# Kernel tuning notes

Hardware: AMD Instinct MI355X
Metric: run time of the kernel (lower is better)

## Reference

```python
import jax, jax.numpy as jnp
import numpy as np

D_MODEL = 1024
N_HEADS = 16
MAX_SEQ_LEN = 2048

def setup_inputs() -> dict:
    key = jax.random.key(0)
    ks = jax.random.split(key, 4)
    B, L, D = 2, 2048, D_MODEL
    s = 0.02
    x = jax.random.normal(ks[0], (B, L, D), dtype=jnp.float32)
    qkv_w = jax.random.normal(ks[1], (D, 3 * D), dtype=jnp.float32) * s
    qkv_b = jnp.zeros((3 * D,), dtype=jnp.float32)
    proj_w = jax.random.normal(ks[2], (D, D), dtype=jnp.float32) * s
    proj_b = jnp.zeros((D,), dtype=jnp.float32)
    bias_table = jax.random.normal(ks[3], (2 * MAX_SEQ_LEN - 1, N_HEADS), dtype=jnp.float32) * s
    return {"x": x, "qkv_w": qkv_w, "qkv_b": qkv_b, "proj_w": proj_w, "proj_b": proj_b, "bias_table": bias_table}

def reference(x, qkv_w, qkv_b, proj_w, proj_b, bias_table):
    B, L, D = x.shape
    H = N_HEADS
    dk = D // H
    scale = dk ** -0.5
    # fused qkv projection: (B,L,3,H,dk)
    qkv = (x @ qkv_w + qkv_b).reshape(B, L, 3, H, dk)
    q = qkv[:, :, 0].transpose(0, 2, 1, 3)  # (B,H,L,dk)
    k = qkv[:, :, 1].transpose(0, 2, 1, 3)
    v = qkv[:, :, 2].transpose(0, 2, 1, 3)
    attn = jnp.einsum("bhqd,bhkd->bhqk", q, k) * scale  # (B,H,L,L)
    # relative position bias gather (Swin-style)
    coords = jnp.arange(L)
    rel_idx = coords[None, :] - coords[:, None] + (MAX_SEQ_LEN - 1)  # (L,L)
    rel_bias = bias_table[rel_idx]  # (L,L,H)
    attn = attn + rel_bias.transpose(2, 0, 1)[None]  # (B,H,L,L)
    attn = jax.nn.softmax(attn, axis=-1)
    out = jnp.einsum("bhqk,bhkd->bhqd", attn, v)  # (B,H,L,dk)
    out = out.transpose(0, 2, 1, 3).reshape(B, L, D)
    return out @ proj_w + proj_b
```

## Files before the change

kernel.cpp:

```cpp
#include <hip/hip_runtime.h>
#include <stdint.h>

typedef __attribute__((ext_vector_type(4))) float    f32x4;
typedef f32x4 __attribute__((aligned(4)))   f32x4u;
typedef __attribute__((ext_vector_type(8))) short    bf16x8;
typedef __attribute__((ext_vector_type(2))) uint32_t u32x2;

#define MFMA16(a,b,c) __builtin_amdgcn_mfma_f32_16x16x32_bf16((a),(b),(c),0,0,0)

__device__ __forceinline__ uint16_t f2bf(float f){
  uint32_t u = __float_as_uint(f);
  return (uint16_t)((u + 0x7FFFu + ((u >> 16) & 1u)) >> 16);
}

__device__ __forceinline__ uint32_t pk_bf16(float lo, float hi){
  uint32_t r; asm("v_cvt_pk_bf16_f32 %0, %1, %2" : "=v"(r) : "v"(lo), "v"(hi)); return r;
}

__device__ __forceinline__ float fast_exp2(float x){
  float r; asm("v_exp_f32 %0, %1" : "=v"(r) : "v"(x)); return r;
}

__device__ __forceinline__ void gload16(const uint16_t* g, uint16_t* l){
  __builtin_amdgcn_global_load_lds((const __attribute__((address_space(1))) uint32_t*)g,
                                   (__attribute__((address_space(3))) uint32_t*)l, 16, 0, 0);
}

__global__ void k_prep(const float* __restrict__ x, uint16_t* __restrict__ x_bf,
                       const float* __restrict__ btab, float* __restrict__ bias_t,
                       const float* __restrict__ qkv_w, uint16_t* __restrict__ qkv_wt,
                       const float* __restrict__ proj_w, uint16_t* __restrict__ proj_wt){
  __shared__ float tile[64][65];
  const int bx = blockIdx.x;
  if (bx < 4096){
    const size_t i = (size_t)(bx*256 + threadIdx.x) * 4;
    const f32x4 v = *(const f32x4*)(x + i);
    u32x2 pk = {pk_bf16(v[0], v[1]), pk_bf16(v[2], v[3])};
    *(u32x2*)(x_bf + i) = pk;
    return;
  }
  if (bx < 4352){
    const int i = (bx - 4096)*256 + threadIdx.x;
    if (i < 4095*16) bias_t[(i & 15)*4096 + (i >> 4)] = btab[i] * 1.4426950408889634f;
    return;
  }
  const float* in;  uint16_t* out;  int K, N, n0, k0;
  if (bx < 5120){
    const int b2 = bx - 4352;
    in = qkv_w; out = qkv_wt; K = 1024; N = 3072;
    n0 = (b2 % 48)*64; k0 = (b2 / 48)*64;
  } else {
    const int b3 = bx - 5120;
    in = proj_w; out = proj_wt; K = 1024; N = 1024;
    n0 = (b3 % 16)*64; k0 = (b3 / 16)*64;
  }
  const int tc = threadIdx.x & 63, tr = threadIdx.x >> 6;
  #pragma unroll
  for (int p=0;p<16;p++){ int r = p*4 + tr; tile[r][tc] = in[(size_t)(k0+r)*N + n0 + tc]; }
  __syncthreads();
  #pragma unroll
  for (int p=0;p<16;p++){ int r = p*4 + tr; out[(size_t)(n0+r)*K + k0 + tc] = f2bf(tile[tc][r]); }
}

__global__ __launch_bounds__(256, 2) void k_gemm(
    const uint16_t* __restrict__ A, const uint16_t* __restrict__ Bt,
    const float* __restrict__ bias,
    uint16_t* __restrict__ qo, uint16_t* __restrict__ ko, uint16_t* __restrict__ vto)
{
  __shared__ __align__(16) uint16_t at[64*64];
  __shared__ __align__(16) uint16_t bt[128*64];
  const int tid = threadIdx.x;
  const int lane = tid & 63, wc = tid >> 6;
  const int g = lane >> 4, li = lane & 15;
  const int m0 = blockIdx.y * 64, n0 = blockIdx.x * 128;

  f32x4 acc[4][2] = {};

  const int srow = tid >> 3;
  const int scg  = (tid & 7) ^ (srow & 7);

  for (int kt_ = 0; kt_ < 16; kt_++){
    const int kk = kt_*64;
    __syncthreads();
    #pragma unroll
    for (int j = 0; j < 2; j++)
      gload16(A  + (size_t)(m0 + j*32 + srow)*1024 + kk + scg*8, at + (j*256+tid)*8);
    #pragma unroll
    for (int j = 0; j < 4; j++)
      gload16(Bt + (size_t)(n0 + j*32 + srow)*1024 + kk + scg*8, bt + (j*256+tid)*8);
    asm volatile("s_waitcnt vmcnt(0)" ::: "memory");
    __syncthreads();

    bf16x8 af[2][4], bfr[2][2];
    #pragma unroll
    for (int mi=0; mi<4; mi++){
      int row = mi*16 + li, sw = row & 7;
      af[0][mi] = *(const bf16x8*)(at + row*64 + ((g     ^ sw)*8));
      af[1][mi] = *(const bf16x8*)(at + row*64 + (((4+g) ^ sw)*8));
    }
    #pragma unroll
    for (int ni=0; ni<2; ni++){
      int row = wc*32 + ni*16 + li, sw = row & 7;
      bfr[0][ni] = *(const bf16x8*)(bt + row*64 + ((g     ^ sw)*8));
      bfr[1][ni] = *(const bf16x8*)(bt + row*64 + (((4+g) ^ sw)*8));
    }
    #pragma unroll
    for (int s=0; s<2; s++)
      #pragma unroll
      for (int mi=0; mi<4; mi++)
        #pragma unroll
        for (int ni=0; ni<2; ni++)
          acc[mi][ni] = MFMA16(af[s][mi], bfr[s][ni], acc[mi][ni]);
  }

  #pragma unroll
  for (int ni=0; ni<2; ni++){
    const int c = n0 + wc*32 + ni*16 + li;
    const float bv = bias[c];
    const int which = c >> 10, cc = c & 1023;
    const int h = cc >> 6, d = cc & 63;
    #pragma unroll
    for (int mi=0; mi<4; mi++){
      const int trow = m0 + mi*16 + g*4;
      const int b_ = trow >> 11, lcl = trow & 2047;
      const f32x4 v4 = acc[mi][ni];
      if (which == 0){
        uint16_t* dst = qo + (((size_t)(b_*16 + h)*2048 + lcl)*64 + d);
        #pragma unroll
        for (int r=0;r<4;r++) dst[(size_t)r*64] = f2bf((v4[r] + bv) * 0.18033688011112042f);
      } else if (which == 1){
        uint16_t* dst = ko + (((size_t)(b_*16 + h)*2048 + lcl)*64 + d);
        #pragma unroll
        for (int r=0;r<4;r++) dst[(size_t)r*64] = f2bf(v4[r] + bv);
      } else {
        u32x2 pk = {pk_bf16(v4[0]+bv, v4[1]+bv), pk_bf16(v4[2]+bv, v4[3]+bv)};
        *(u32x2*)(vto + (((size_t)(b_*16 + h)*64 + d)*2048 + lcl)) = pk;
      }
    }
  }
}

__global__ __launch_bounds__(256, 2) void k_gemm2(
    const uint16_t* __restrict__ A, const uint16_t* __restrict__ Bt,
    const float* __restrict__ bias, float* __restrict__ outf)
{
  __shared__ __align__(16) uint16_t at[128*64];
  __shared__ __align__(16) uint16_t bt[64*64];
  const int tid = threadIdx.x;
  const int lane = tid & 63, w = tid >> 6;
  const int g = lane >> 4, li = lane & 15;
  const int wr = w >> 1, wc = w & 1;
  const int m0 = blockIdx.y * 128, n0 = blockIdx.x * 64;

  f32x4 acc[4][2] = {};
  const int srow = tid >> 3;
  const int scg  = (tid & 7) ^ (srow & 7);

  for (int kt_ = 0; kt_ < 16; kt_++){
    const int kk = kt_*64;
    __syncthreads();
    #pragma unroll
    for (int j = 0; j < 4; j++)
      gload16(A  + (size_t)(m0 + j*32 + srow)*1024 + kk + scg*8, at + (j*256+tid)*8);
    #pragma unroll
    for (int j = 0; j < 2; j++)
      gload16(Bt + (size_t)(n0 + j*32 + srow)*1024 + kk + scg*8, bt + (j*256+tid)*8);
    asm volatile("s_waitcnt vmcnt(0)" ::: "memory");
    __syncthreads();

    bf16x8 af[2][4], bfr[2][2];
    #pragma unroll
    for (int mi=0; mi<4; mi++){
      int row = wr*64 + mi*16 + li, sw = row & 7;
      af[0][mi] = *(const bf16x8*)(at + row*64 + ((g     ^ sw)*8));
      af[1][mi] = *(const bf16x8*)(at + row*64 + (((4+g) ^ sw)*8));
    }
    #pragma unroll
    for (int ni=0; ni<2; ni++){
      int row = wc*32 + ni*16 + li, sw = row & 7;
      bfr[0][ni] = *(const bf16x8*)(bt + row*64 + ((g     ^ sw)*8));
      bfr[1][ni] = *(const bf16x8*)(bt + row*64 + (((4+g) ^ sw)*8));
    }
    #pragma unroll
    for (int s=0; s<2; s++)
      #pragma unroll
      for (int mi=0; mi<4; mi++)
        #pragma unroll
        for (int ni=0; ni<2; ni++)
          acc[mi][ni] = MFMA16(af[s][mi], bfr[s][ni], acc[mi][ni]);
  }

  #pragma unroll
  for (int ni=0; ni<2; ni++){
    const int c = n0 + wc*32 + ni*16 + li;
    const float bv = bias[c];
    #pragma unroll
    for (int mi=0; mi<4; mi++){
      const int trow = m0 + wr*64 + mi*16 + g*4;
      float* dst = outf + (size_t)trow*1024 + c;
      const f32x4 v4 = acc[mi][ni];
      #pragma unroll
      for (int r=0;r<4;r++) dst[(size_t)r*1024] = v4[r] + bv;
    }
  }
}

__device__ __forceinline__ void attn_tile(
    int t, bool last, int tid, int g, int li, int srow, int scg,
    const uint16_t* kbase, const uint16_t* vbase, const float* bb,
    const uint16_t* ktc, uint16_t* ktn, const uint16_t* vtc, uint16_t* vtn, uint16_t* pl,
    const bf16x8 (&qf)[2][2], bf16x8 ones,
    f32x4 (&o)[4][2], f32x4 (&o4)[2], float& mrun0, float& mrun1)
{
  const int kv0 = t*64;

  f32x4 bv5[5];
  #pragma unroll
  for (int j=0;j<5;j++)
    bv5[j] = *(const f32x4u*)(bb + kv0 + (j-1)*16 + g*4 - li);
  asm volatile("" ::: "memory");

  if (!last){
    const int kv1 = kv0 + 64;
    gload16(kbase + (size_t)(kv1+srow)*64 + scg*8,         ktn + tid*8);
    gload16(kbase + (size_t)(kv1+srow+32)*64 + scg*8,      ktn + 2048 + tid*8);
    gload16(vbase + (size_t)srow*2048 + kv1 + scg*8,       vtn + tid*8);
    gload16(vbase + (size_t)(srow+32)*2048 + kv1 + scg*8,  vtn + 2048 + tid*8);
    asm volatile("s_waitcnt vmcnt(9)" ::: "memory");
  } else {
    asm volatile("s_waitcnt vmcnt(5)" ::: "memory");
  }
  __builtin_amdgcn_s_barrier();

  f32x4 sa[4][2];
  __builtin_amdgcn_s_setprio(1);
  #pragma unroll
  for (int mf=0; mf<4; mf++){
    const int row = mf*16 + li, sw = row & 7;
    bf16x8 a0 = *(const bf16x8*)(ktc + row*64 + ((g     ^ sw)*8));
    bf16x8 a1 = *(const bf16x8*)(ktc + row*64 + (((4+g) ^ sw)*8));
    #pragma unroll
    for (int c=0;c<2;c++){
      f32x4 cfr = {};
      cfr = MFMA16(a0, qf[c][0], cfr);
      cfr = MFMA16(a1, qf[c][1], cfr);
      sa[mf][c] = cfr;
    }
  }
  __builtin_amdgcn_s_setprio(0);

  float t0 = -__builtin_inff(), t1 = -__builtin_inff();
  #pragma unroll
  for (int mf=0; mf<4; mf++){
    sa[mf][0] += bv5[mf+1];
    sa[mf][1] += bv5[mf];
    #pragma unroll
    for (int r=0; r<4; r++){
      t0 = fmaxf(t0, sa[mf][0][r]);
      t1 = fmaxf(t1, sa[mf][1][r]);
    }
  }

  const int ok = (t0 <= mrun0 + 8.f) && (t1 <= mrun1 + 8.f);
  if (!__all(ok)){
    float r0 = t0, r1 = t1;
    r0 = fmaxf(r0, __shfl_xor(r0, 16)); r0 = fmaxf(r0, __shfl_xor(r0, 32));
    r1 = fmaxf(r1, __shfl_xor(r1, 16)); r1 = fmaxf(r1, __shfl_xor(r1, 32));
    const float mn0 = fmaxf(mrun0, r0), mn1 = fmaxf(mrun1, r1);
    const float a0 = fast_exp2(mrun0 - mn0), a1 = fast_exp2(mrun1 - mn1);
    #pragma unroll
    for (int mf=0; mf<4; mf++){ o[mf][0] *= a0; o[mf][1] *= a1; }
    o4[0] *= a0; o4[1] *= a1;
    mrun0 = mn0; mrun1 = mn1;
  }

  bf16x8 av[2][4];
  #pragma unroll
  for (int s=0; s<2; s++)
    #pragma unroll
    for (int mf=0; mf<4; mf++){
      const int row = mf*16 + li, sw = row & 7;
      av[s][mf] = *(const bf16x8*)(vtc + row*64 + (((4*s+g) ^ sw)*8));
    }

  const int swp2 = 2*(li & 7);
  #pragma unroll
  for (int c=0;c<2;c++){
    const float mr = c ? mrun1 : mrun0;
    #pragma unroll
    for (int mf=0; mf<4; mf++){
      float p0 = fast_exp2(sa[mf][c][0] - mr);
      float p1 = fast_exp2(sa[mf][c][1] - mr);
      float p2 = fast_exp2(sa[mf][c][2] - mr);
      float p3 = fast_exp2(sa[mf][c][3] - mr);
      u32x2 pk = {pk_bf16(p0,p1), pk_bf16(p2,p3)};
      *(u32x2*)(pl + li*64 + (((4*mf+g) ^ swp2)*4)) = pk;
    }
    __builtin_amdgcn_s_setprio(1);
    #pragma unroll
    for (int s=0; s<2; s++){
      bf16x8 pb = *(const bf16x8*)(pl + li*64 + (((8*s+2*g) ^ swp2)*4));
      o4[c] = MFMA16(ones, pb, o4[c]);
      #pragma unroll
      for (int mf=0; mf<4; mf++)
        o[mf][c] = MFMA16(av[s][mf], pb, o[mf][c]);
    }
    __builtin_amdgcn_s_setprio(0);
  }
  __builtin_amdgcn_s_barrier();
}

__global__ __launch_bounds__(256, 2) void k_attn(
    const uint16_t* __restrict__ qg, const uint16_t* __restrict__ kg,
    const uint16_t* __restrict__ vg, const float* __restrict__ biast,
    uint16_t* __restrict__ outp)
{
  __shared__ __align__(16) uint16_t kt[2][64*64];
  __shared__ __align__(16) uint16_t vt[2][64*64];
  __shared__ __align__(16) uint16_t pt[4][16*64];
  const int tid = threadIdx.x;
  const int lane = tid & 63, w = tid >> 6;
  const int g = lane >> 4, li = lane & 15;
  const int bh = blockIdx.y, h = bh & 15, b_ = bh >> 4;
  const int qw = blockIdx.x*128 + w*32;

  bf16x8 qf[2][2];
  #pragma unroll
  for (int c=0;c<2;c++){
    const uint16_t* qp = qg + ((size_t)bh*2048 + qw + c*16 + li)*64 + g*8;
    qf[c][0] = *(const bf16x8*)(qp);
    qf[c][1] = *(const bf16x8*)(qp + 32);
  }
  bf16x8 ones = (bf16x8)(short)0;
  if (li == 0){ const short v = (short)0x3F80; ones = (bf16x8){v,v,v,v,v,v,v,v}; }

  f32x4 o[4][2] = {};
  f32x4 o4[2] = {};
  float mrun0 = -__builtin_inff(), mrun1 = -__builtin_inff();

  const uint16_t* kbase = kg + (size_t)bh*(2048*64);
  const uint16_t* vbase = vg + (size_t)bh*(64*2048);
  const int srow = tid >> 3;
  const int scg  = (tid & 7) ^ (srow & 7);
  const float* bb = biast + h*4096 + 2047 - qw;
  uint16_t* pl = &pt[w][0];

  gload16(kbase + (size_t)srow*64 + scg*8,         &kt[0][tid*8]);
  gload16(kbase + (size_t)(srow+32)*64 + scg*8,    &kt[0][2048 + tid*8]);
  gload16(vbase + (size_t)srow*2048 + scg*8,       &vt[0][tid*8]);
  gload16(vbase + (size_t)(srow+32)*2048 + scg*8,  &vt[0][2048 + tid*8]);

  for (int tt = 0; tt < 32; tt += 2){
    attn_tile(tt,   false,    tid, g, li, srow, scg, kbase, vbase, bb,
              &kt[0][0], &kt[1][0], &vt[0][0], &vt[1][0], pl,
              qf, ones, o, o4, mrun0, mrun1);
    attn_tile(tt+1, tt == 30, tid, g, li, srow, scg, kbase, vbase, bb,
              &kt[1][0], &kt[0][0], &vt[1][0], &vt[0][0], pl,
              qf, ones, o, o4, mrun0, mrun1);
  }

  const float ls0 = __shfl(o4[0][0], li);
  const float ls1 = __shfl(o4[1][0], li);
  const float inv0 = 1.0f / ls0, inv1 = 1.0f / ls1;
  #pragma unroll
  for (int c=0;c<2;c++){
    const float inv = c ? inv1 : inv0;
    const size_t token = (size_t)b_*2048 + qw + c*16 + li;
    #pragma unroll
    for (int mf=0; mf<4; mf++){
      u32x2 pk = {pk_bf16(o[mf][c][0]*inv, o[mf][c][1]*inv),
                  pk_bf16(o[mf][c][2]*inv, o[mf][c][3]*inv)};
      *(u32x2*)(outp + token*1024 + h*64 + mf*16 + g*4) = pk;
    }
  }
}

extern "C" void kernel_launch(void* const* d_in, const int* in_sizes, int n_in,
                              void* d_out, int out_size, void* d_ws, size_t ws_size,
                              hipStream_t stream)
{
  const float* x      = (const float*)d_in[0];
  const float* qkv_w  = (const float*)d_in[1];
  const float* qkv_b  = (const float*)d_in[2];
  const float* proj_w = (const float*)d_in[3];
  const float* proj_b = (const float*)d_in[4];
  const float* btab   = (const float*)d_in[5];
  float* out = (float*)d_out;

  char* p = (char*)d_ws;
  uint16_t* x_bf    = (uint16_t*)(p);
  uint16_t* qkv_wt  = (uint16_t*)(p + 8388608);
  uint16_t* proj_wt = (uint16_t*)(p + 14680064);
  uint16_t* q_buf   = (uint16_t*)(p + 16777216);
  uint16_t* k_buf   = (uint16_t*)(p + 25165824);
  uint16_t* vt_buf  = (uint16_t*)(p + 33554432);
  uint16_t* ao_buf  = (uint16_t*)(p + 41943040);
  float*    bias_t  = (float*)   (p + 50331648);

  k_prep <<<dim3(5376), dim3(256), 0, stream>>>(x, x_bf, btab, bias_t,
                                                qkv_w, qkv_wt, proj_w, proj_wt);

  k_gemm  <<<dim3(24,64), dim3(256), 0, stream>>>(x_bf, qkv_wt, qkv_b, q_buf, k_buf, vt_buf);
  k_attn  <<<dim3(16,32), dim3(256), 0, stream>>>(q_buf, k_buf, vt_buf, bias_t, ao_buf);
  k_gemm2 <<<dim3(16,32), dim3(256), 0, stream>>>(ao_buf, proj_wt, proj_b, out);
}
```

Measured before the change: 118.0 us.

## Switch attention kernel to 32x32x16 MFMA with register-resident P via cross-lane shuffles

Rewrites the attention inner loop to use 32x32x16 bf16 MFMA, so each wave computes S and O for 32 queries with two 16-wide accumulator tiles. The probabilities are repacked across the half-waves with shuffles and fed straight back as the B operand, which removes the per-wave LDS P buffer and its write/read round trip. The row sum is now accumulated in registers instead of through an extra MFMA against a ones vector. The wait counts change to match the new number of bias loads, and the register footprint per lane changes, which may affect occupancy.

```diff
diff --git a/kernel.cpp b/kernel.cpp
--- a/kernel.cpp
+++ b/kernel.cpp
@@ -1,12 +1,15 @@
 #include <hip/hip_runtime.h>
 #include <stdint.h>
 
-typedef __attribute__((ext_vector_type(4))) float    f32x4;
-typedef f32x4 __attribute__((aligned(4)))   f32x4u;
-typedef __attribute__((ext_vector_type(8))) short    bf16x8;
-typedef __attribute__((ext_vector_type(2))) uint32_t u32x2;
+typedef __attribute__((ext_vector_type(4)))  float    f32x4;
+typedef f32x4 __attribute__((aligned(4)))    f32x4u;
+typedef __attribute__((ext_vector_type(16))) float    f32x16;
+typedef __attribute__((ext_vector_type(8)))  short    bf16x8;
+typedef __attribute__((ext_vector_type(2)))  uint32_t u32x2;
+typedef __attribute__((ext_vector_type(4)))  uint32_t u32x4;
 
 #define MFMA16(a,b,c) __builtin_amdgcn_mfma_f32_16x16x32_bf16((a),(b),(c),0,0,0)
+#define MFMA32(a,b,c) __builtin_amdgcn_mfma_f32_32x32x16_bf16((a),(b),(c),0,0,0)
 
 __device__ __forceinline__ uint16_t f2bf(float f){
   uint32_t u = __float_as_uint(f);
@@ -25,6 +28,8 @@
   __builtin_amdgcn_global_load_lds((const __attribute__((address_space(1))) uint32_t*)g,
                                    (__attribute__((address_space(3))) uint32_t*)l, 16, 0, 0);
 }
+
+typedef union { u32x4 u; bf16x8 b; } pun_t;
 
 __global__ void k_prep(const float* __restrict__ x, uint16_t* __restrict__ x_bf,
                        const float* __restrict__ btab, float* __restrict__ bias_t,
@@ -206,18 +211,20 @@
 }
 
 __device__ __forceinline__ void attn_tile(
-    int t, bool last, int tid, int g, int li, int srow, int scg,
-    const uint16_t* kbase, const uint16_t* vbase, const float* bb,
-    const uint16_t* ktc, uint16_t* ktn, const uint16_t* vtc, uint16_t* vtn, uint16_t* pl,
-    const bf16x8 (&qf)[2][2], bf16x8 ones,
-    f32x4 (&o)[4][2], f32x4 (&o4)[2], float& mrun0, float& mrun1)
+    int t, bool last, int tid, int l31, int h, int srow, int scg,
+    const uint16_t* kbase, const uint16_t* vbase, const float* bbl,
+    const uint16_t* ktc, uint16_t* ktn, const uint16_t* vtc, uint16_t* vtn,
+    const bf16x8 (&qf)[4],
+    f32x16& o0, f32x16& o1, float& mrun, float& lrun)
 {
   const int kv0 = t*64;
 
-  f32x4 bv5[5];
-  #pragma unroll
-  for (int j=0;j<5;j++)
-    bv5[j] = *(const f32x4u*)(bb + kv0 + (j-1)*16 + g*4 - li);
+  f32x4 bv0[4], bv1[4];
+  #pragma unroll
+  for (int q2=0;q2<4;q2++){
+    bv0[q2] = *(const f32x4u*)(bbl + kv0 + 8*q2);
+    bv1[q2] = *(const f32x4u*)(bbl + kv0 + 32 + 8*q2);
+  }
   asm volatile("" ::: "memory");
 
   if (!last){
@@ -226,87 +233,75 @@
     gload16(kbase + (size_t)(kv1+srow+32)*64 + scg*8,      ktn + 2048 + tid*8);
     gload16(vbase + (size_t)srow*2048 + kv1 + scg*8,       vtn + tid*8);
     gload16(vbase + (size_t)(srow+32)*2048 + kv1 + scg*8,  vtn + 2048 + tid*8);
-    asm volatile("s_waitcnt vmcnt(9)" ::: "memory");
+    asm volatile("s_waitcnt vmcnt(12)" ::: "memory");
   } else {
-    asm volatile("s_waitcnt vmcnt(5)" ::: "memory");
+    asm volatile("s_waitcnt vmcnt(8)" ::: "memory");
   }
   __builtin_amdgcn_s_barrier();
 
-  f32x4 sa[4][2];
+  const int sw = l31 & 7;
+  f32x16 sA = {}, sB = {};
   __builtin_amdgcn_s_setprio(1);
   #pragma unroll
-  for (int mf=0; mf<4; mf++){
-    const int row = mf*16 + li, sw = row & 7;
-    bf16x8 a0 = *(const bf16x8*)(ktc + row*64 + ((g     ^ sw)*8));
-    bf16x8 a1 = *(const bf16x8*)(ktc + row*64 + (((4+g) ^ sw)*8));
-    #pragma unroll
-    for (int c=0;c<2;c++){
-      f32x4 cfr = {};
-      cfr = MFMA16(a0, qf[c][0], cfr);
-      cfr = MFMA16(a1, qf[c][1], cfr);
-      sa[mf][c] = cfr;
-    }
+  for (int s=0;s<4;s++){
+    const int ch = (((2*s+h) ^ sw))*8;
+    bf16x8 a0 = *(const bf16x8*)(ktc + l31*64 + ch);
+    bf16x8 a1 = *(const bf16x8*)(ktc + (32+l31)*64 + ch);
+    sA = MFMA32(a0, qf[s], sA);
+    sB = MFMA32(a1, qf[s], sB);
   }
   __builtin_amdgcn_s_setprio(0);
 
-  float t0 = -__builtin_inff(), t1 = -__builtin_inff();
-  #pragma unroll
-  for (int mf=0; mf<4; mf++){
-    sa[mf][0] += bv5[mf+1];
-    sa[mf][1] += bv5[mf];
-    #pragma unroll
-    for (int r=0; r<4; r++){
-      t0 = fmaxf(t0, sa[mf][0][r]);
-      t1 = fmaxf(t1, sa[mf][1][r]);
-    }
-  }
-
-  const int ok = (t0 <= mrun0 + 8.f) && (t1 <= mrun1 + 8.f);
+  float tmax = -__builtin_inff();
+  #pragma unroll
+  for (int r=0;r<16;r++){
+    sA[r] += bv0[r>>2][r&3];
+    sB[r] += bv1[r>>2][r&3];
+    tmax = fmaxf(tmax, fmaxf(sA[r], sB[r]));
+  }
+  tmax = fmaxf(tmax, __shfl_xor(tmax, 32));
+
+  const int ok = (tmax <= mrun + 8.f);
   if (!__all(ok)){
-    float r0 = t0, r1 = t1;
-    r0 = fmaxf(r0, __shfl_xor(r0, 16)); r0 = fmaxf(r0, __shfl_xor(r0, 32));
-    r1 = fmaxf(r1, __shfl_xor(r1, 16)); r1 = fmaxf(r1, __shfl_xor(r1, 32));
-    const float mn0 = fmaxf(mrun0, r0), mn1 = fmaxf(mrun1, r1);
-    const float a0 = fast_exp2(mrun0 - mn0), a1 = fast_exp2(mrun1 - mn1);
-    #pragma unroll
-    for (int mf=0; mf<4; mf++){ o[mf][0] *= a0; o[mf][1] *= a1; }
-    o4[0] *= a0; o4[1] *= a1;
-    mrun0 = mn0; mrun1 = mn1;
-  }
-
-  bf16x8 av[2][4];
-  #pragma unroll
-  for (int s=0; s<2; s++)
-    #pragma unroll
-    for (int mf=0; mf<4; mf++){
-      const int row = mf*16 + li, sw = row & 7;
-      av[s][mf] = *(const bf16x8*)(vtc + row*64 + (((4*s+g) ^ sw)*8));
-    }
-
-  const int swp2 = 2*(li & 7);
-  #pragma unroll
-  for (int c=0;c<2;c++){
-    const float mr = c ? mrun1 : mrun0;
-    #pragma unroll
-    for (int mf=0; mf<4; mf++){
-      float p0 = fast_exp2(sa[mf][c][0] - mr);
-      float p1 = fast_exp2(sa[mf][c][1] - mr);
-      float p2 = fast_exp2(sa[mf][c][2] - mr);
-      float p3 = fast_exp2(sa[mf][c][3] - mr);
-      u32x2 pk = {pk_bf16(p0,p1), pk_bf16(p2,p3)};
-      *(u32x2*)(pl + li*64 + (((4*mf+g) ^ swp2)*4)) = pk;
-    }
-    __builtin_amdgcn_s_setprio(1);
-    #pragma unroll
-    for (int s=0; s<2; s++){
-      bf16x8 pb = *(const bf16x8*)(pl + li*64 + (((8*s+2*g) ^ swp2)*4));
-      o4[c] = MFMA16(ones, pb, o4[c]);
-      #pragma unroll
-      for (int mf=0; mf<4; mf++)
-        o[mf][c] = MFMA16(av[s][mf], pb, o[mf][c]);
-    }
-    __builtin_amdgcn_s_setprio(0);
-  }
+    const float mn = fmaxf(mrun, tmax);
+    const float al = fast_exp2(mrun - mn);
+    #pragma unroll
+    for (int r=0;r<16;r++){ o0[r] *= al; o1[r] *= al; }
+    lrun *= al; mrun = mn;
+  }
+
+  float psum = 0.f;
+  uint32_t pkA[8], pkB[8];
+  #pragma unroll
+  for (int m=0;m<4;m++){
+    float a0 = fast_exp2(sA[4*m+0]-mrun), a1 = fast_exp2(sA[4*m+1]-mrun);
+    float a2 = fast_exp2(sA[4*m+2]-mrun), a3 = fast_exp2(sA[4*m+3]-mrun);
+    float b0 = fast_exp2(sB[4*m+0]-mrun), b1 = fast_exp2(sB[4*m+1]-mrun);
+    float b2 = fast_exp2(sB[4*m+2]-mrun), b3 = fast_exp2(sB[4*m+3]-mrun);
+    psum += ((a0+a1)+(a2+a3)) + ((b0+b1)+(b2+b3));
+    pkA[2*m] = pk_bf16(a0,a1); pkA[2*m+1] = pk_bf16(a2,a3);
+    pkB[2*m] = pk_bf16(b0,b1); pkB[2*m+1] = pk_bf16(b2,b3);
+  }
+  lrun += psum;
+
+  __builtin_amdgcn_s_setprio(1);
+  #pragma unroll
+  for (int s=0;s<4;s++){
+    const uint32_t* pks = (s < 2) ? pkA : pkB;
+    const int sl = s & 1;
+    const uint32_t c0 = pks[4*sl], c1 = pks[4*sl+1], c2 = pks[4*sl+2], c3 = pks[4*sl+3];
+    const uint32_t v0 = h ? c0 : c2, v1 = h ? c1 : c3;
+    const uint32_t r0 = (uint32_t)__shfl_xor((int)v0, 32);
+    const uint32_t r1 = (uint32_t)__shfl_xor((int)v1, 32);
+    pun_t pn;
+    pn.u = (u32x4){ h ? r0 : c0, h ? r1 : c1, h ? c2 : r0, h ? c3 : r1 };
+    const int ch = (((2*s+h) ^ sw))*8;
+    bf16x8 av0 = *(const bf16x8*)(vtc + l31*64 + ch);
+    bf16x8 av1 = *(const bf16x8*)(vtc + (32+l31)*64 + ch);
+    o0 = MFMA32(av0, pn.b, o0);
+    o1 = MFMA32(av1, pn.b, o1);
+  }
+  __builtin_amdgcn_s_setprio(0);
   __builtin_amdgcn_s_barrier();
 }
 
@@ -317,33 +312,28 @@
 {
   __shared__ __align__(16) uint16_t kt[2][64*64];
   __shared__ __align__(16) uint16_t vt[2][64*64];
-  __shared__ __align__(16) uint16_t pt[4][16*64];
   const int tid = threadIdx.x;
   const int lane = tid & 63, w = tid >> 6;
-  const int g = lane >> 4, li = lane & 15;
-  const int bh = blockIdx.y, h = bh & 15, b_ = bh >> 4;
+  const int l31 = lane & 31, h = lane >> 5;
+  const int bh = blockIdx.y, h_head = bh & 15, b_ = bh >> 4;
   const int qw = blockIdx.x*128 + w*32;
-
-  bf16x8 qf[2][2];
-  #pragma unroll
-  for (int c=0;c<2;c++){
-    const uint16_t* qp = qg + ((size_t)bh*2048 + qw + c*16 + li)*64 + g*8;
-    qf[c][0] = *(const bf16x8*)(qp);
-    qf[c][1] = *(const bf16x8*)(qp + 32);
-  }
-  bf16x8 ones = (bf16x8)(short)0;
-  if (li == 0){ const short v = (short)0x3F80; ones = (bf16x8){v,v,v,v,v,v,v,v}; }
-
-  f32x4 o[4][2] = {};
-  f32x4 o4[2] = {};
-  float mrun0 = -__builtin_inff(), mrun1 = -__builtin_inff();
+  const int q_tok = qw + l31;
+
+  bf16x8 qf[4];
+  {
+    const uint16_t* qp = qg + ((size_t)bh*2048 + q_tok)*64 + h*8;
+    #pragma unroll
+    for (int s=0;s<4;s++) qf[s] = *(const bf16x8*)(qp + s*16);
+  }
+
+  f32x16 o0 = {}, o1 = {};
+  float mrun = -__builtin_inff(), lrun = 0.f;
 
   const uint16_t* kbase = kg + (size_t)bh*(2048*64);
   const uint16_t* vbase = vg + (size_t)bh*(64*2048);
   const int srow = tid >> 3;
   const int scg  = (tid & 7) ^ (srow & 7);
-  const float* bb = biast + h*4096 + 2047 - qw;
-  uint16_t* pl = &pt[w][0];
+  const float* bbl = biast + h_head*4096 + 2047 - q_tok + 4*h;
 
   gload16(kbase + (size_t)srow*64 + scg*8,         &kt[0][tid*8]);
   gload16(kbase + (size_t)(srow+32)*64 + scg*8,    &kt[0][2048 + tid*8]);
@@ -351,27 +341,22 @@
   gload16(vbase + (size_t)(srow+32)*2048 + scg*8,  &vt[0][2048 + tid*8]);
 
   for (int tt = 0; tt < 32; tt += 2){
-    attn_tile(tt,   false,    tid, g, li, srow, scg, kbase, vbase, bb,
-              &kt[0][0], &kt[1][0], &vt[0][0], &vt[1][0], pl,
-              qf, ones, o, o4, mrun0, mrun1);
-    attn_tile(tt+1, tt == 30, tid, g, li, srow, scg, kbase, vbase, bb,
-              &kt[1][0], &kt[0][0], &vt[1][0], &vt[0][0], pl,
-              qf, ones, o, o4, mrun0, mrun1);
-  }
-
-  const float ls0 = __shfl(o4[0][0], li);
-  const float ls1 = __shfl(o4[1][0], li);
-  const float inv0 = 1.0f / ls0, inv1 = 1.0f / ls1;
-  #pragma unroll
-  for (int c=0;c<2;c++){
-    const float inv = c ? inv1 : inv0;
-    const size_t token = (size_t)b_*2048 + qw + c*16 + li;
-    #pragma unroll
-    for (int mf=0; mf<4; mf++){
-      u32x2 pk = {pk_bf16(o[mf][c][0]*inv, o[mf][c][1]*inv),
-                  pk_bf16(o[mf][c][2]*inv, o[mf][c][3]*inv)};
-      *(u32x2*)(outp + token*1024 + h*64 + mf*16 + g*4) = pk;
-    }
+    attn_tile(tt,   false,    tid, l31, h, srow, scg, kbase, vbase, bbl,
+              &kt[0][0], &kt[1][0], &vt[0][0], &vt[1][0], qf, o0, o1, mrun, lrun);
+    attn_tile(tt+1, tt == 30, tid, l31, h, srow, scg, kbase, vbase, bbl,
+              &kt[1][0], &kt[0][0], &vt[1][0], &vt[0][0], qf, o0, o1, mrun, lrun);
+  }
+
+  const float ls = lrun + __shfl_xor(lrun, 32);
+  const float inv = 1.0f / ls;
+  const size_t token = (size_t)b_*2048 + q_tok;
+  uint16_t* dst = outp + token*1024 + h_head*64 + 4*h;
+  #pragma unroll
+  for (int q2=0;q2<4;q2++){
+    u32x2 w0 = {pk_bf16(o0[4*q2]*inv, o0[4*q2+1]*inv), pk_bf16(o0[4*q2+2]*inv, o0[4*q2+3]*inv)};
+    *(u32x2*)(dst + 8*q2) = w0;
+    u32x2 w1 = {pk_bf16(o1[4*q2]*inv, o1[4*q2+1]*inv), pk_bf16(o1[4*q2+2]*inv, o1[4*q2+3]*inv)};
+    *(u32x2*)(dst + 32 + 8*q2) = w1;
   }
 }
 
```

New measurement: 122.1 us. 3.4% more time.
